# Performance work log

Measured on AMD Instinct MI355X. Metric: run time of the kernel, lower is better.

The kernel has to match this reference:

```python
import jax, jax.numpy as jnp
import numpy as np
from jax import lax

# geomloss SamplesLoss('sinkhorn', p=2, blur=0.01, scaling=0.9) semantics:
# debiased Sinkhorn divergence S_eps(a,b) = OT_eps(x,y) - 0.5*OT_eps(x,x) - 0.5*OT_eps(y,y)
# with cost C = ||x-y||^2 / 2, uniform weights, and epsilon annealing from
# diameter^p down to blur^p with ratio scaling^p.
P = 2
BLUR = 0.01
SCALING = 0.9
DIAMETER = 8.0  # static upper bound on point-cloud spread for randn data

def _eps_schedule():
    scales = []
    s = DIAMETER
    while s > BLUR:
        scales.append(s)
        s *= SCALING
    scales.append(BLUR)
    return jnp.asarray(np.array(scales, np.float32) ** P)

def _sqcost(x, y):
    # x: [B,N,D], y: [B,M,D] -> C[B,N,M] = 0.5*||x_i-y_j||^2
    x2 = jnp.sum(x * x, -1)[:, :, None]
    y2 = jnp.sum(y * y, -1)[:, None, :]
    return 0.5 * (x2 + y2 - 2.0 * jnp.einsum('bnd,bmd->bnm', x, y))

def _sinkhorn_divergence(x, y):
    B, N, _ = x.shape
    M = y.shape[1]
    logN = jnp.log(jnp.float32(N))
    logM = jnp.log(jnp.float32(M))
    eps_list = _eps_schedule()

    Cxy = _sqcost(x, y)          # [B,N,M]
    Cyx = jnp.swapaxes(Cxy, 1, 2)
    Cxx = _sqcost(x, x)
    Cyy = _sqcost(y, y)

    def softmin(eps, C, h, logw):
        # -eps * log sum_j exp(log w_j + (h_j - C_ij)/eps)
        return -eps * jax.nn.logsumexp((h[:, None, :] - C) / eps - logw, axis=-1)

    # potentials computed under envelope theorem (no grad through iterations)
    Cxy_d, Cyx_d = lax.stop_gradient(Cxy), lax.stop_gradient(Cyx)
    Cxx_d, Cyy_d = lax.stop_gradient(Cxx), lax.stop_gradient(Cyy)

    z = jnp.zeros((B, N), x.dtype)
    zy = jnp.zeros((B, M), x.dtype)

    def body(carry, eps):
        f, g, fx, gy = carry
        ft = softmin(eps, Cxy_d, g, logM)
        gt = softmin(eps, Cyx_d, f, logN)
        f, g = 0.5 * (f + ft), 0.5 * (g + gt)
        fx = 0.5 * (fx + softmin(eps, Cxx_d, fx, logN))
        gy = 0.5 * (gy + softmin(eps, Cyy_d, gy, logM))
        return (f, g, fx, gy), None

    (f, g, fx, gy), _ = lax.scan(body, (z, zy, z, zy), eps_list)

    # last extrapolation at target eps, differentiable w.r.t. the costs
    eps_t = eps_list[-1]
    f_fin = softmin(eps_t, Cxy, lax.stop_gradient(g), logM)
    g_fin = softmin(eps_t, Cyx, lax.stop_gradient(f), logN)
    fx_fin = softmin(eps_t, Cxx, lax.stop_gradient(fx), logN)
    gy_fin = softmin(eps_t, Cyy, lax.stop_gradient(gy), logM)

    # S = <a, f - fx> + <b, g - gy>, uniform weights
    return jnp.mean(f_fin - fx_fin, axis=-1) + jnp.mean(g_fin - gy_fin, axis=-1)  # [B]


def setup_inputs() -> dict:
    key = jax.random.key(0)
    k1, k2 = jax.random.split(key)
    B, N, D = 8, 2048, 3
    p1 = jax.random.normal(k1, (B, N, D), dtype=jnp.float32)
    p2 = jax.random.normal(k2, (B, N, D), dtype=jnp.float32)
    return {"p1": p1, "p2": p2}


def reference(p1, p2):
    # EMD_Loss.forward: mean over batch of per-sample Sinkhorn divergences
    return jnp.mean(_sinkhorn_divergence(p1, p2))
```

## Files before the change

kernel.cpp:

```cpp
#include <hip/hip_runtime.h>
#include <math.h>

#define NPTS 2048
#define NB 8
#define R 2
#define NW 16
#define BROWS 128
#define CPAIR 64

typedef float v2f __attribute__((ext_vector_type(2)));

__device__ __forceinline__ float wexp2(float v) { return __builtin_amdgcn_exp2f(v); }
__device__ __forceinline__ v2f fma2(v2f a, v2f b, v2f c) {
  return __builtin_elementwise_fma(a, b, c);
}
__device__ __forceinline__ v2f max2(v2f a, v2f b) {
  return __builtin_elementwise_max(a, b);
}

__global__ __launch_bounds__(256) void emd_init(const float* __restrict__ x,
                                                const float* __restrict__ y,
                                                float4* __restrict__ x4,
                                                float4* __restrict__ y4,
                                                float* __restrict__ pot0,
                                                float* __restrict__ out) {
  int t = blockIdx.x * blockDim.x + threadIdx.x;
  if (t < NB * NPTS) {
    float a0 = x[3 * t], a1 = x[3 * t + 1], a2 = x[3 * t + 2];
    x4[t] = make_float4(a0, a1, a2, 0.5f * (a0 * a0 + a1 * a1 + a2 * a2));
    float b0 = y[3 * t], b1 = y[3 * t + 1], b2 = y[3 * t + 2];
    y4[t] = make_float4(b0, b1, b2, 0.5f * (b0 * b0 + b1 * b1 + b2 * b2));
  }
  pot0[t] = 0.0f;
  if (t == 0) out[0] = 0.0f;
}


__global__ __launch_bounds__(1024, 8) void emd_sweep_boot(
    const float4* __restrict__ x4, const float4* __restrict__ y4,
    const float* __restrict__ pot_in, float* __restrict__ pot_out,
    float* __restrict__ amax_out, float c, float neg_eps_ln2, float eps_logM) {
  __shared__ union {
    struct {
      float4 A[NPTS / 2];
      float4 B[NPTS / 2];
    } cp;
    struct {
      float m[NW][BROWS];
      float l[NW][BROWS];
    } mg;
  } sh;

  int blk = blockIdx.x;
  int mat = blk >> 7;
  int b = (blk >> 4) & 7;
  int rg = blk & 15;
  int tid = threadIdx.x;
  int lane = tid & 63;
  int w = tid >> 6;

  const float4* rowp = (mat == 1 || mat == 3) ? y4 : x4;
  const float4* colp = (mat == 0 || mat == 3) ? y4 : x4;
  int hidx = (mat < 2) ? (mat ^ 1) : mat;
  const float* h = pot_in + (hidx * NB + b) * NPTS;
  const float4* colb = colp + b * NPTS;

  {
    float4 q0 = colb[2 * tid];
    float4 q1 = colb[2 * tid + 1];
    float2 hv = ((const float2*)h)[tid];
    sh.cp.A[tid] = make_float4(q0.x, q1.x, q0.y, q1.y);
    sh.cp.B[tid] = make_float4(q0.z, q1.z, (hv.x - q0.w) * c, (hv.y - q1.w) * c);
  }
  __syncthreads();

  int rowbase = rg * BROWS;
  const float4* rowb = rowp + b * NPTS + rowbase;

  v2f xs0[R], xs1[R], xs2[R];
  float m[R], l[R];
#pragma unroll
  for (int r = 0; r < R; ++r) {
    float4 p = rowb[r * 64 + lane];
    float a0 = p.x * c, a1 = p.y * c, a2 = p.z * c;
    xs0[r] = (v2f){a0, a0};
    xs1[r] = (v2f){a1, a1};
    xs2[r] = (v2f){a2, a2};
    m[r] = -INFINITY;
    l[r] = 0.0f;
  }

  int p0 = w * CPAIR;
  for (int tp = 0; tp < CPAIR; tp += 4) {
    float4 A[4], B[4];
#pragma unroll
    for (int j = 0; j < 4; ++j) {
      A[j] = sh.cp.A[p0 + tp + j];
      B[j] = sh.cp.B[p0 + tp + j];
    }
#pragma unroll
    for (int r = 0; r < R; ++r) {
      v2f s2[4];
#pragma unroll
      for (int j = 0; j < 4; ++j) {
        v2f qx = {A[j].x, A[j].y};
        v2f qy = {A[j].z, A[j].w};
        v2f qz = {B[j].x, B[j].y};
        v2f qw = {B[j].z, B[j].w};
        s2[j] = fma2(xs0[r], qx, fma2(xs1[r], qy, fma2(xs2[r], qz, qw)));
      }
      v2f t0 = max2(s2[0], s2[1]);
      v2f t1 = max2(s2[2], s2[3]);
      v2f u = max2(t0, t1);
      float mt = fmaxf(u.x, u.y);
      float mn = fmaxf(m[r], mt);
      v2f mn2 = {mn, mn};
      v2f acc = {0.0f, 0.0f};
#pragma unroll
      for (int j = 0; j < 4; ++j) {
        v2f d = s2[j] - mn2;
        v2f e;
        e.x = wexp2(d.x);
        e.y = wexp2(d.y);
        acc += e;
      }
      float er = wexp2(m[r] - mn);
      l[r] = fmaf(l[r], er, acc.x + acc.y);
      m[r] = mn;
    }
  }

  __syncthreads();
#pragma unroll
  for (int r = 0; r < R; ++r) {
    sh.mg.m[w][r * 64 + lane] = m[r];
    sh.mg.l[w][r * 64 + lane] = l[r];
  }
  __syncthreads();

  if (w < 2) {
    int row = w * 64 + lane;
    float M = sh.mg.m[0][row];
#pragma unroll
    for (int q = 1; q < NW; ++q) M = fmaxf(M, sh.mg.m[q][row]);
    float L = 0.0f;
#pragma unroll
    for (int q = 0; q < NW; ++q)
      L += sh.mg.l[q][row] * wexp2(sh.mg.m[q][row] - M);
    float pw = rowb[row].w;
    float res = pw + neg_eps_ln2 * (M + log2f(L)) + eps_logM;
    float invc = -neg_eps_ln2;
    amax_out[(mat * NB + b) * NPTS + rowbase + row] = M * invc;
    const float* oldp = pot_in + (mat * NB + b) * NPTS + rowbase;
    float* outp = pot_out + (mat * NB + b) * NPTS + rowbase;
    outp[row] = 0.5f * (oldp[row] + res);
  }
}

template <bool FINAL>
__global__ __launch_bounds__(1024, 8) void emd_sweep_ref(
    const float4* __restrict__ x4, const float4* __restrict__ y4,
    const float* __restrict__ pot_in, float* __restrict__ pot_out,
    const float* __restrict__ amax_in, float* __restrict__ amax_out,
    float* __restrict__ out, float c, float neg_eps_ln2, float eps_logM) {
  __shared__ union {
    struct {
      float4 A[NPTS / 2];
      float4 B[NPTS / 2];
    } cp;
    float lbuf[NW][BROWS];
  } sh;

  int blk = blockIdx.x;
  int mat = blk >> 7;
  int b = (blk >> 4) & 7;
  int rg = blk & 15;
  int tid = threadIdx.x;
  int lane = tid & 63;
  int w = tid >> 6;

  const float4* rowp = (mat == 1 || mat == 3) ? y4 : x4;
  const float4* colp = (mat == 0 || mat == 3) ? y4 : x4;
  int hidx = (mat < 2) ? (mat ^ 1) : mat;
  const float* h = pot_in + (hidx * NB + b) * NPTS;
  const float4* colb = colp + b * NPTS;

  {
    float4 q0 = colb[2 * tid];
    float4 q1 = colb[2 * tid + 1];
    float2 hv = ((const float2*)h)[tid];
    sh.cp.A[tid] = make_float4(q0.x, q1.x, q0.y, q1.y);
    sh.cp.B[tid] = make_float4(q0.z, q1.z, (hv.x - q0.w) * c, (hv.y - q1.w) * c);
  }

  int rowbase = rg * BROWS;
  const float4* rowb = rowp + b * NPTS + rowbase;
  const float* amrow = amax_in + (mat * NB + b) * NPTS + rowbase;

  v2f xs0[R], xs1[R], xs2[R], mref2[R], acc[R];
#pragma unroll
  for (int r = 0; r < R; ++r) {
    float4 p = rowb[r * 64 + lane];
    float a0 = p.x * c, a1 = p.y * c, a2 = p.z * c;
    xs0[r] = (v2f){a0, a0};
    xs1[r] = (v2f){a1, a1};
    xs2[r] = (v2f){a2, a2};
    float mr = amrow[r * 64 + lane] * c;
    mref2[r] = (v2f){mr, mr};
    acc[r] = (v2f){0.0f, 0.0f};
  }
  __syncthreads();

  int p0 = w * CPAIR;
  for (int tp = 0; tp < CPAIR; tp += 4) {
    float4 A[4], B[4];
#pragma unroll
    for (int j = 0; j < 4; ++j) {
      A[j] = sh.cp.A[p0 + tp + j];
      B[j] = sh.cp.B[p0 + tp + j];
    }
#pragma unroll
    for (int r = 0; r < R; ++r) {
#pragma unroll
      for (int j = 0; j < 4; ++j) {
        v2f qx = {A[j].x, A[j].y};
        v2f qy = {A[j].z, A[j].w};
        v2f qz = {B[j].x, B[j].y};
        v2f qw = {B[j].z, B[j].w};
        v2f s2 = fma2(xs0[r], qx, fma2(xs1[r], qy, fma2(xs2[r], qz, qw)));
        v2f d = s2 - mref2[r];
        v2f e;
        e.x = wexp2(d.x);
        e.y = wexp2(d.y);
        acc[r] += e;
      }
    }
  }

  __syncthreads();
#pragma unroll
  for (int r = 0; r < R; ++r)
    sh.lbuf[w][r * 64 + lane] = acc[r].x + acc[r].y;
  __syncthreads();

  if (w < 2) {
    int row = w * 64 + lane;
    float L = sh.lbuf[0][row];
#pragma unroll
    for (int q = 1; q < NW; ++q) L += sh.lbuf[q][row];
    float mr = amrow[row] * c;
    float lse = mr + log2f(L);
    float pw = rowb[row].w;
    float res = pw + neg_eps_ln2 * lse + eps_logM;
    float invc = -neg_eps_ln2;
    if (FINAL) {
      float sign = (mat < 2) ? 1.0f : -1.0f;
      float val = sign * res * (1.0f / (float)(NB * NPTS));
#pragma unroll
      for (int off = 32; off; off >>= 1) val += __shfl_xor(val, off);
      if (lane == 0) atomicAdd(out, val);
    } else {
      amax_out[(mat * NB + b) * NPTS + rowbase + row] = lse * invc;
      const float* oldp = pot_in + (mat * NB + b) * NPTS + rowbase;
      float* outp = pot_out + (mat * NB + b) * NPTS + rowbase;
      outp[row] = 0.5f * (oldp[row] + res);
    }
  }
}

extern "C" void kernel_launch(void* const* d_in, const int* in_sizes, int n_in,
                              void* d_out, int out_size, void* d_ws, size_t ws_size,
                              hipStream_t stream) {
  const float* x = (const float*)d_in[0];
  const float* y = (const float*)d_in[1];
  float* out = (float*)d_out;

  char* ws = (char*)d_ws;
  float4* x4 = (float4*)ws;
  float4* y4 = (float4*)(ws + 262144);
  float* pot = (float*)(ws + 524288);
  float* amax = (float*)(ws + 1048576);

  emd_init<<<256, 256, 0, stream>>>(x, y, x4, y4, pot, out);

  float eps_arr[80];
  int ne = 0;
  double s = 8.0;
  while (s > 0.01) {
    float sf = (float)s;
    eps_arr[ne++] = sf * sf;
    s *= 0.9;
  }
  {
    float bf = 0.01f;
    eps_arr[ne++] = bf * bf;
  }

  const double LOG2E = 1.4426950408889634;
  const double LN2 = 0.6931471805599453;
  const double LOG2048 = 7.624618986159398;

  int cur = 0;
  for (int k = 0; k < ne; ++k) {
    float eps = eps_arr[k];
    float c = (float)(LOG2E / (double)eps);
    float nel = (float)(-(double)eps * LN2);
    float elM = (float)((double)eps * LOG2048);
    if (k == 0) {
      emd_sweep_boot<<<512, 1024, 0, stream>>>(x4, y4, pot + cur * 65536,
                                               pot + (1 - cur) * 65536, amax,
                                               c, nel, elM);
    } else {
      emd_sweep_ref<false><<<512, 1024, 0, stream>>>(
          x4, y4, pot + cur * 65536, pot + (1 - cur) * 65536, amax, amax, out,
          c, nel, elM);
    }
    cur ^= 1;
  }

  {
    float eps = eps_arr[ne - 1];
    float c = (float)(LOG2E / (double)eps);
    float nel = (float)(-(double)eps * LN2);
    float elM = (float)((double)eps * LOG2048);
    emd_sweep_ref<true><<<512, 1024, 0, stream>>>(
        x4, y4, pot + cur * 65536, nullptr, amax, nullptr, out, c, nel, elM);
  }
}
```

Before: 1.378 ms.

## Split sweep into column-half partial kernel plus separate merge kernel

Replaces the fused per-iteration sweep kernel with two kernels. A partial kernel gives each block 256 rows and half of the columns, with 4 rows per thread so each shared-memory column pair is reused across more rows, and writes partial sums to a buffer. A small merge kernel then combines the two halves, takes the log-sum-exp and updates the potentials. The goal is more register-level reuse of the loaded column data per exp/FMA, at the cost of an extra launch per iteration, extra global traffic for the partial sums, and double-buffered amax arrays.

Result: slower. 1.574 ms (+14.3%).

```diff
diff --git a/kernel.cpp b/kernel.cpp
--- a/kernel.cpp
+++ b/kernel.cpp
@@ -3,10 +3,6 @@
 
 #define NPTS 2048
 #define NB 8
-#define R 2
-#define NW 16
-#define BROWS 128
-#define CPAIR 64
 
 typedef float v2f __attribute__((ext_vector_type(2)));
 
@@ -35,20 +31,13 @@
   if (t == 0) out[0] = 0.0f;
 }
 
-
 __global__ __launch_bounds__(1024, 8) void emd_sweep_boot(
     const float4* __restrict__ x4, const float4* __restrict__ y4,
     const float* __restrict__ pot_in, float* __restrict__ pot_out,
     float* __restrict__ amax_out, float c, float neg_eps_ln2, float eps_logM) {
   __shared__ union {
-    struct {
-      float4 A[NPTS / 2];
-      float4 B[NPTS / 2];
-    } cp;
-    struct {
-      float m[NW][BROWS];
-      float l[NW][BROWS];
-    } mg;
+    struct { float4 A[NPTS / 2]; float4 B[NPTS / 2]; } cp;
+    struct { float m[16][128]; float l[16][128]; } mg;
   } sh;
 
   int blk = blockIdx.x;
@@ -59,7 +48,7 @@
   int lane = tid & 63;
   int w = tid >> 6;
 
-  const float4* rowp = (mat == 1 || mat == 3) ? y4 : x4;
+  const float4* rowp = (mat & 1) ? y4 : x4;
   const float4* colp = (mat == 0 || mat == 3) ? y4 : x4;
   int hidx = (mat < 2) ? (mat ^ 1) : mat;
   const float* h = pot_in + (hidx * NB + b) * NPTS;
@@ -74,13 +63,13 @@
   }
   __syncthreads();
 
-  int rowbase = rg * BROWS;
+  int rowbase = rg * 128;
   const float4* rowb = rowp + b * NPTS + rowbase;
 
-  v2f xs0[R], xs1[R], xs2[R];
-  float m[R], l[R];
-#pragma unroll
-  for (int r = 0; r < R; ++r) {
+  v2f xs0[2], xs1[2], xs2[2];
+  float m[2], l[2];
+#pragma unroll
+  for (int r = 0; r < 2; ++r) {
     float4 p = rowb[r * 64 + lane];
     float a0 = p.x * c, a1 = p.y * c, a2 = p.z * c;
     xs0[r] = (v2f){a0, a0};
@@ -90,8 +79,8 @@
     l[r] = 0.0f;
   }
 
-  int p0 = w * CPAIR;
-  for (int tp = 0; tp < CPAIR; tp += 4) {
+  int p0 = w * 64;
+  for (int tp = 0; tp < 64; tp += 4) {
     float4 A[4], B[4];
 #pragma unroll
     for (int j = 0; j < 4; ++j) {
@@ -99,7 +88,7 @@
       B[j] = sh.cp.B[p0 + tp + j];
     }
 #pragma unroll
-    for (int r = 0; r < R; ++r) {
+    for (int r = 0; r < 2; ++r) {
       v2f s2[4];
 #pragma unroll
       for (int j = 0; j < 4; ++j) {
@@ -124,15 +113,14 @@
         e.y = wexp2(d.y);
         acc += e;
       }
-      float er = wexp2(m[r] - mn);
-      l[r] = fmaf(l[r], er, acc.x + acc.y);
+      l[r] = fmaf(l[r], wexp2(m[r] - mn), acc.x + acc.y);
       m[r] = mn;
     }
   }
 
   __syncthreads();
 #pragma unroll
-  for (int r = 0; r < R; ++r) {
+  for (int r = 0; r < 2; ++r) {
     sh.mg.m[w][r * 64 + lane] = m[r];
     sh.mg.l[w][r * 64 + lane] = l[r];
   }
@@ -142,64 +130,61 @@
     int row = w * 64 + lane;
     float M = sh.mg.m[0][row];
 #pragma unroll
-    for (int q = 1; q < NW; ++q) M = fmaxf(M, sh.mg.m[q][row]);
+    for (int q = 1; q < 16; ++q) M = fmaxf(M, sh.mg.m[q][row]);
     float L = 0.0f;
 #pragma unroll
-    for (int q = 0; q < NW; ++q)
+    for (int q = 0; q < 16; ++q)
       L += sh.mg.l[q][row] * wexp2(sh.mg.m[q][row] - M);
     float pw = rowb[row].w;
     float res = pw + neg_eps_ln2 * (M + log2f(L)) + eps_logM;
     float invc = -neg_eps_ln2;
-    amax_out[(mat * NB + b) * NPTS + rowbase + row] = M * invc;
-    const float* oldp = pot_in + (mat * NB + b) * NPTS + rowbase;
-    float* outp = pot_out + (mat * NB + b) * NPTS + rowbase;
-    outp[row] = 0.5f * (oldp[row] + res);
-  }
-}
-
-template <bool FINAL>
-__global__ __launch_bounds__(1024, 8) void emd_sweep_ref(
+    int idx = (mat * NB + b) * NPTS + rowbase + row;
+    amax_out[idx] = M * invc;
+    pot_out[idx] = 0.5f * (pot_in[idx] + res);
+  }
+}
+
+__global__ __launch_bounds__(1024, 8) void emd_partial(
     const float4* __restrict__ x4, const float4* __restrict__ y4,
-    const float* __restrict__ pot_in, float* __restrict__ pot_out,
-    const float* __restrict__ amax_in, float* __restrict__ amax_out,
-    float* __restrict__ out, float c, float neg_eps_ln2, float eps_logM) {
+    const float* __restrict__ pot_in, const float* __restrict__ am_in,
+    float* __restrict__ Lp, float c) {
   __shared__ union {
-    struct {
-      float4 A[NPTS / 2];
-      float4 B[NPTS / 2];
-    } cp;
-    float lbuf[NW][BROWS];
+    struct { float4 A[512]; float4 B[512]; } cp;
+    float lbuf[16][256];
   } sh;
 
   int blk = blockIdx.x;
   int mat = blk >> 7;
   int b = (blk >> 4) & 7;
-  int rg = blk & 15;
+  int rg = (blk >> 1) & 7;
+  int cg = blk & 1;
   int tid = threadIdx.x;
   int lane = tid & 63;
   int w = tid >> 6;
 
-  const float4* rowp = (mat == 1 || mat == 3) ? y4 : x4;
+  const float4* rowp = (mat & 1) ? y4 : x4;
   const float4* colp = (mat == 0 || mat == 3) ? y4 : x4;
   int hidx = (mat < 2) ? (mat ^ 1) : mat;
   const float* h = pot_in + (hidx * NB + b) * NPTS;
   const float4* colb = colp + b * NPTS;
 
-  {
-    float4 q0 = colb[2 * tid];
-    float4 q1 = colb[2 * tid + 1];
-    float2 hv = ((const float2*)h)[tid];
+  if (tid < 512) {
+    int jg = cg * 1024 + 2 * tid;
+    float4 q0 = colb[jg];
+    float4 q1 = colb[jg + 1];
+    float2 hv = *(const float2*)(h + jg);
     sh.cp.A[tid] = make_float4(q0.x, q1.x, q0.y, q1.y);
     sh.cp.B[tid] = make_float4(q0.z, q1.z, (hv.x - q0.w) * c, (hv.y - q1.w) * c);
   }
-
-  int rowbase = rg * BROWS;
+  __syncthreads();
+
+  int rowbase = rg * 256;
   const float4* rowb = rowp + b * NPTS + rowbase;
-  const float* amrow = amax_in + (mat * NB + b) * NPTS + rowbase;
-
-  v2f xs0[R], xs1[R], xs2[R], mref2[R], acc[R];
-#pragma unroll
-  for (int r = 0; r < R; ++r) {
+  const float* amrow = am_in + (mat * NB + b) * NPTS + rowbase;
+
+  v2f xs0[4], xs1[4], xs2[4], mref2[4], acc[4];
+#pragma unroll
+  for (int r = 0; r < 4; ++r) {
     float4 p = rowb[r * 64 + lane];
     float a0 = p.x * c, a1 = p.y * c, a2 = p.z * c;
     xs0[r] = (v2f){a0, a0};
@@ -209,62 +194,67 @@
     mref2[r] = (v2f){mr, mr};
     acc[r] = (v2f){0.0f, 0.0f};
   }
-  __syncthreads();
-
-  int p0 = w * CPAIR;
-  for (int tp = 0; tp < CPAIR; tp += 4) {
-    float4 A[4], B[4];
-#pragma unroll
-    for (int j = 0; j < 4; ++j) {
-      A[j] = sh.cp.A[p0 + tp + j];
-      B[j] = sh.cp.B[p0 + tp + j];
+
+  int p0 = w * 32;
+  for (int tp = 0; tp < 32; ++tp) {
+    float4 A = sh.cp.A[p0 + tp];
+    float4 B = sh.cp.B[p0 + tp];
+    v2f qx = {A.x, A.y};
+    v2f qy = {A.z, A.w};
+    v2f qz = {B.x, B.y};
+    v2f qw = {B.z, B.w};
+#pragma unroll
+    for (int r = 0; r < 4; ++r) {
+      v2f s2 = fma2(xs0[r], qx, fma2(xs1[r], qy, fma2(xs2[r], qz, qw)));
+      v2f d = s2 - mref2[r];
+      v2f e;
+      e.x = wexp2(d.x);
+      e.y = wexp2(d.y);
+      acc[r] += e;
     }
-#pragma unroll
-    for (int r = 0; r < R; ++r) {
-#pragma unroll
-      for (int j = 0; j < 4; ++j) {
-        v2f qx = {A[j].x, A[j].y};
-        v2f qy = {A[j].z, A[j].w};
-        v2f qz = {B[j].x, B[j].y};
-        v2f qw = {B[j].z, B[j].w};
-        v2f s2 = fma2(xs0[r], qx, fma2(xs1[r], qy, fma2(xs2[r], qz, qw)));
-        v2f d = s2 - mref2[r];
-        v2f e;
-        e.x = wexp2(d.x);
-        e.y = wexp2(d.y);
-        acc[r] += e;
-      }
-    }
-  }
-
-  __syncthreads();
-#pragma unroll
-  for (int r = 0; r < R; ++r)
+  }
+
+  __syncthreads();
+#pragma unroll
+  for (int r = 0; r < 4; ++r)
     sh.lbuf[w][r * 64 + lane] = acc[r].x + acc[r].y;
   __syncthreads();
 
-  if (w < 2) {
+  if (w < 4) {
     int row = w * 64 + lane;
     float L = sh.lbuf[0][row];
 #pragma unroll
-    for (int q = 1; q < NW; ++q) L += sh.lbuf[q][row];
-    float mr = amrow[row] * c;
-    float lse = mr + log2f(L);
-    float pw = rowb[row].w;
-    float res = pw + neg_eps_ln2 * lse + eps_logM;
-    float invc = -neg_eps_ln2;
-    if (FINAL) {
-      float sign = (mat < 2) ? 1.0f : -1.0f;
-      float val = sign * res * (1.0f / (float)(NB * NPTS));
-#pragma unroll
-      for (int off = 32; off; off >>= 1) val += __shfl_xor(val, off);
-      if (lane == 0) atomicAdd(out, val);
-    } else {
-      amax_out[(mat * NB + b) * NPTS + rowbase + row] = lse * invc;
-      const float* oldp = pot_in + (mat * NB + b) * NPTS + rowbase;
-      float* outp = pot_out + (mat * NB + b) * NPTS + rowbase;
-      outp[row] = 0.5f * (oldp[row] + res);
-    }
+    for (int q = 1; q < 16; ++q) L += sh.lbuf[q][row];
+    Lp[2 * ((mat * NB + b) * NPTS) + cg * NPTS + rowbase + row] = L;
+  }
+}
+
+template <bool FINAL>
+__global__ __launch_bounds__(256) void emd_merge(
+    const float4* __restrict__ x4, const float4* __restrict__ y4,
+    const float* __restrict__ Lp, const float* __restrict__ am_in,
+    const float* __restrict__ pot_in, float* __restrict__ pot_out,
+    float* __restrict__ am_out, float* __restrict__ out,
+    float invc, float elM) {
+  int t = blockIdx.x * 256 + threadIdx.x;
+  int mat = t >> 14;
+  int b = (t >> 11) & 7;
+  int i = t & 2047;
+  const float4* rowp = (mat & 1) ? y4 : x4;
+  float pw = rowp[b * NPTS + i].w;
+  int base = (mat * NB + b) * NPTS;
+  float L = Lp[2 * base + i] + Lp[2 * base + NPTS + i];
+  float lse = fmaf(log2f(L), invc, am_in[base + i]);
+  float res = pw - lse + elM;
+  if (FINAL) {
+    float sign = (mat < 2) ? 1.0f : -1.0f;
+    float val = sign * res * (1.0f / (float)(NB * NPTS));
+#pragma unroll
+    for (int off = 32; off; off >>= 1) val += __shfl_xor(val, off);
+    if ((threadIdx.x & 63) == 0) atomicAdd(out, val);
+  } else {
+    pot_out[base + i] = 0.5f * (pot_in[base + i] + res);
+    am_out[base + i] = lse;
   }
 }
 
@@ -279,7 +269,10 @@
   float4* x4 = (float4*)ws;
   float4* y4 = (float4*)(ws + 262144);
   float* pot = (float*)(ws + 524288);
-  float* amax = (float*)(ws + 1048576);
+  float* am[2];
+  am[0] = (float*)(ws + 1048576);
+  am[1] = (float*)(ws + 1310720);
+  float* Lp = (float*)(ws + 1572864);
 
   emd_init<<<256, 256, 0, stream>>>(x, y, x4, y4, pot, out);
 
@@ -300,30 +293,38 @@
   const double LN2 = 0.6931471805599453;
   const double LOG2048 = 7.624618986159398;
 
-  int cur = 0;
-  for (int k = 0; k < ne; ++k) {
-    float eps = eps_arr[k];
+  {
+    float eps = eps_arr[0];
     float c = (float)(LOG2E / (double)eps);
     float nel = (float)(-(double)eps * LN2);
     float elM = (float)((double)eps * LOG2048);
-    if (k == 0) {
-      emd_sweep_boot<<<512, 1024, 0, stream>>>(x4, y4, pot + cur * 65536,
-                                               pot + (1 - cur) * 65536, amax,
-                                               c, nel, elM);
-    } else {
-      emd_sweep_ref<false><<<512, 1024, 0, stream>>>(
-          x4, y4, pot + cur * 65536, pot + (1 - cur) * 65536, amax, amax, out,
-          c, nel, elM);
-    }
-    cur ^= 1;
+    emd_sweep_boot<<<512, 1024, 0, stream>>>(x4, y4, pot, pot + 65536,
+                                             am[0], c, nel, elM);
+  }
+
+  for (int k = 1; k < ne; ++k) {
+    float eps = eps_arr[k];
+    float c = (float)(LOG2E / (double)eps);
+    float invc = (float)((double)eps * LN2);
+    float elM = (float)((double)eps * LOG2048);
+    float* potIn = pot + (k % 2) * 65536;
+    float* potOut = pot + ((k + 1) % 2) * 65536;
+    const float* amIn = am[(k - 1) % 2];
+    float* amOut = am[k % 2];
+    emd_partial<<<512, 1024, 0, stream>>>(x4, y4, potIn, amIn, Lp, c);
+    emd_merge<false><<<256, 256, 0, stream>>>(x4, y4, Lp, amIn, potIn, potOut,
+                                              amOut, nullptr, invc, elM);
   }
 
   {
     float eps = eps_arr[ne - 1];
     float c = (float)(LOG2E / (double)eps);
-    float nel = (float)(-(double)eps * LN2);
+    float invc = (float)((double)eps * LN2);
     float elM = (float)((double)eps * LOG2048);
-    emd_sweep_ref<true><<<512, 1024, 0, stream>>>(
-        x4, y4, pot + cur * 65536, nullptr, amax, nullptr, out, c, nel, elM);
-  }
-}
+    float* potIn = pot + (ne % 2) * 65536;
+    const float* amIn = am[(ne - 1) % 2];
+    emd_partial<<<512, 1024, 0, stream>>>(x4, y4, potIn, amIn, Lp, c);
+    emd_merge<true><<<256, 256, 0, stream>>>(x4, y4, Lp, amIn, nullptr, nullptr,
+                                             nullptr, out, invc, elM);
+  }
+}
```
